# Optimization experiments

Measured on AMD Instinct MI355X. Metric: run time of the kernel, lower is better.

Reference implementation:

```python
import jax, jax.numpy as jnp
import numpy as np

N_BOXES = 2048
N_CLASSES = 20


def _cross(a, b):
    return a[..., 0] * b[..., 1] - a[..., 1] * b[..., 0]


def _corners(box):
    # box: [5] = cx, cy, w, h, angle -> [4,2] corner coords
    cx, cy, w, h, a = box[0], box[1], box[2], box[3], box[4]
    c, s = jnp.cos(a), jnp.sin(a)
    dx = jnp.array([-1.0, 1.0, 1.0, -1.0], box.dtype) * (w * 0.5)
    dy = jnp.array([-1.0, -1.0, 1.0, 1.0], box.dtype) * (h * 0.5)
    return jnp.stack([cx + c * dx - s * dy, cy + s * dx + c * dy], axis=-1)


def _points_in_box(pts, box):
    # pts [K,2]; rotate into box frame, test axis-aligned containment
    cx, cy, w, h, a = box[0], box[1], box[2], box[3], box[4]
    c, s = jnp.cos(a), jnp.sin(a)
    px = pts[:, 0] - cx
    py = pts[:, 1] - cy
    lx = c * px + s * py
    ly = -s * px + c * py
    eps = 1e-5
    return (jnp.abs(lx) <= w * 0.5 + eps) & (jnp.abs(ly) <= h * 0.5 + eps)


def _pair_inter_area(box_a, box_b):
    # Exact convex intersection area of two rotated rectangles.
    ca = _corners(box_a)
    cb = _corners(box_b)
    # all 4x4 edge-pair intersections
    p = ca[:, None, :]
    r = (jnp.roll(ca, -1, 0) - ca)[:, None, :]
    q = cb[None, :, :]
    s_ = (jnp.roll(cb, -1, 0) - cb)[None, :, :]
    denom = _cross(r, s_)
    qp = q - p
    safe = jnp.where(jnp.abs(denom) > 1e-9, denom, 1.0)
    t = _cross(qp, s_) / safe
    u = _cross(qp, r) / safe
    valid_e = (jnp.abs(denom) > 1e-9) & (t >= 0.0) & (t <= 1.0) & (u >= 0.0) & (u <= 1.0)
    ipts = p + t[..., None] * r  # [4,4,2]
    # candidate polygon vertices: corners of A in B, corners of B in A, edge crossings
    pts = jnp.concatenate([ca, cb, ipts.reshape(16, 2)], axis=0)  # [24,2]
    mask = jnp.concatenate([_points_in_box(ca, box_b), _points_in_box(cb, box_a), valid_e.reshape(16)], axis=0)
    k = jnp.sum(mask)
    m = mask.astype(pts.dtype)[:, None]
    center = jnp.sum(pts * m, axis=0) / jnp.maximum(k, 1).astype(pts.dtype)
    d = pts - center
    ang = jnp.where(mask, jnp.arctan2(d[:, 1], d[:, 0]), 1e9)  # invalid -> sorted last
    idx = jnp.argsort(ang)
    ds = d[idx]
    ar = jnp.arange(24)
    nxt = jnp.where(ar + 1 < k, ar + 1, 0)
    cr = _cross(ds, ds[nxt])
    area = 0.5 * jnp.abs(jnp.sum(jnp.where(ar < k, cr, 0.0)))
    return jnp.where(k >= 3, area, 0.0)


def _iou_one_vs_many(box, boxes):
    inter = jax.vmap(lambda b: _pair_inter_area(box, b))(boxes)  # [N]
    area_a = box[2] * box[3]
    area_b = boxes[:, 2] * boxes[:, 3]
    return inter / (area_a + area_b - inter + 1e-9)


def _rotated_nms_mask(boxes, scores, iou_threshold):
    # sequential greedy suppression, highest score first; returns bool keep mask (original order)
    n = boxes.shape[0]
    order = jnp.argsort(-scores)
    bs = boxes[order]
    ar = jnp.arange(n)

    def body(i, keep):
        ious = _iou_one_vs_many(bs[i], bs)
        suppress = (ious > iou_threshold) & (ar > i) & keep[i]
        return keep & ~suppress

    keep_sorted = jax.lax.fori_loop(0, n, body, jnp.ones((n,), bool))
    return jnp.zeros((n,), bool).at[order].set(keep_sorted)


def setup_inputs() -> dict:
    key = jax.random.key(0)
    k1, k2, k3, k4, k5 = jax.random.split(key, 5)
    cxcy = jax.random.uniform(k1, (N_BOXES, 2), jnp.float32) * 1024.0
    wh = jax.random.uniform(k2, (N_BOXES, 2), jnp.float32) * 96.0 + 4.0
    ang = jax.random.uniform(k3, (N_BOXES, 1), jnp.float32) * np.pi
    boxes = jnp.concatenate([cxcy, wh, ang], axis=1)  # [N,5]
    scores = jax.random.uniform(k4, (N_BOXES,), jnp.float32)
    labels = jax.random.randint(k5, (N_BOXES,), 0, N_CLASSES, dtype=jnp.int64 if jax.config.read('jax_enable_x64') else jnp.int32)
    return {"boxes": boxes, "scores": scores, "labels": labels, "iou_threshold": 0.5}


def reference(boxes, scores, labels, iou_threshold):
    # multiclass NMS via coordinate-offset trick (N <= 20000 branch of forward)
    cx, cy, w, h = boxes[:, 0], boxes[:, 1], boxes[:, 2], boxes[:, 3]
    max_radius = jnp.max(jnp.sqrt(w * w + h * h)) * 0.5
    max_coord = jnp.maximum(jnp.max(cx), jnp.max(cy))
    offset_scale = (max_coord + max_radius) * 2.0 + 1.0
    offsets = labels.astype(boxes.dtype) * offset_scale
    boxes_nms = boxes.at[:, 0].add(offsets).at[:, 1].add(offsets)
    keep = _rotated_nms_mask(boxes_nms, scores, iou_threshold)
    # fixed-shape encoding of the kept-index set: score of kept boxes, 0 for suppressed
    return scores * keep.astype(scores.dtype)
```

## Files before the change

kernel.cpp:

```cpp
#include <hip/hip_runtime.h>
#include <cstdint>

typedef unsigned long long u64;
typedef uint32_t u32;

#define NB 2048
#define NBLK 256
#define SLICE 512
#define CLIST_CAP 2048
#define GCOMP_CAP 131072
#define MAGIC 0x9E3779B1u


__global__ __launch_bounds__(256) void nms_fused_kernel(
    const float* __restrict__ boxes, const float* __restrict__ scores,
    const int* __restrict__ labels, const float* __restrict__ thrp,
    u32* __restrict__ edges, u32* __restrict__ cntA, u32* __restrict__ tagA,
    u32* __restrict__ gcomp, float* __restrict__ out) {
#pragma clang fp contract(off)
  __shared__ float sc[NB];
  __shared__ float smc[4], smr[4];
  __shared__ u32 clist[CLIST_CAP];
  __shared__ float dxL[256 * 25];
  __shared__ float dyL[256 * 25];
  __shared__ u32 ccnt;
  __shared__ u32 ecntL;
  __shared__ u32 cntL[NBLK];
  __shared__ u32 sA[NBLK];
  __shared__ u64 keepw[32];
  __shared__ u32 Sw32[64];
  __shared__ int changed;
  int t = threadIdx.x;
  int b = blockIdx.x;
  if (t == 0) { ccnt = 0; ecntL = 0; }
  float mc = -1e30f, mr = -1e30f;
  for (int k = t; k < NB; k += 256) {
    float cx = boxes[k * 5 + 0];
    float cy = boxes[k * 5 + 1];
    float w = boxes[k * 5 + 2];
    float h = boxes[k * 5 + 3];
    mc = fmaxf(mc, fmaxf(cx, cy));
    float ww = w * w;
    float hh = h * h;
    mr = fmaxf(mr, sqrtf(ww + hh));
    sc[k] = scores[k];
  }
  for (int off = 32; off > 0; off >>= 1) {
    mc = fmaxf(mc, __shfl_down(mc, off));
    mr = fmaxf(mr, __shfl_down(mr, off));
  }
  if ((t & 63) == 0) { smc[t >> 6] = mc; smr[t >> 6] = mr; }
  __syncthreads();
  mc = fmaxf(fmaxf(smc[0], smc[1]), fmaxf(smc[2], smc[3]));
  mr = fmaxf(fmaxf(smr[0], smr[1]), fmaxf(smr[2], smr[3]));
  float osc = (mc + mr * 0.5f) * 2.0f + 1.0f;

  float jx[8], jy[8], jr[8];
#pragma unroll
  for (int c = 0; c < 8; ++c) {
    int j = c * 256 + t;
    float off = (float)labels[j] * osc;
    float w = boxes[j * 5 + 2];
    float h = boxes[j * 5 + 3];
    float ww = w * w;
    float hh = h * h;
    jx[c] = boxes[j * 5 + 0] + off;
    jy[c] = boxes[j * 5 + 1] + off;
    jr[c] = 0.5f * sqrtf(ww + hh);
  }
  int i0 = b * 8;
#pragma unroll
  for (int di = 0; di < 8; ++di) {
    int i = i0 + di;
    float offi = (float)labels[i] * osc;
    float wI = boxes[i * 5 + 2];
    float hI = boxes[i * 5 + 3];
    float wwI = wI * wI;
    float hhI = hI * hI;
    float ax = boxes[i * 5 + 0] + offi;
    float ay = boxes[i * 5 + 1] + offi;
    float ar = 0.5f * sqrtf(wwI + hhI);
#pragma unroll
    for (int c = 0; c < 8; ++c) {
      int j = c * 256 + t;
      if (j > i) {
        float dx = jx[c] - ax, dy = jy[c] - ay;
        float rr = ar + jr[c] + 1.0f;
        if (dx * dx + dy * dy <= rr * rr) {
          u32 s = atomicAdd(&ccnt, 1u);
          if (s < CLIST_CAP) clist[s] = ((u32)i << 16) | (u32)j;
        }
      }
    }
  }
  __syncthreads();
  u32 cnt = ccnt < CLIST_CAP ? ccnt : CLIST_CAP;
  float thr = *thrp;
  u32* myEdges = edges + (u32)b * SLICE;
  float* myDx = &dxL[t * 25];
  float* myDy = &dyL[t * 25];
  for (u32 idx = t; idx < cnt; idx += 256) {
    u32 pk = clist[idx];
    int bi = (int)(pk >> 16);
    int bj = (int)(pk & 0xFFFFu);
    float offa = (float)labels[bi] * osc;
    float acx = boxes[bi * 5 + 0] + offa;
    float acy = boxes[bi * 5 + 1] + offa;
    float aw = boxes[bi * 5 + 2];
    float ah = boxes[bi * 5 + 3];
    float aang = boxes[bi * 5 + 4];
    float ac = cosf(aang);
    float as_ = sinf(aang);
    float offb = (float)labels[bj] * osc;
    float bcx = boxes[bj * 5 + 0] + offb;
    float bcy = boxes[bj * 5 + 1] + offb;
    float bw = boxes[bj * 5 + 2];
    float bh = boxes[bj * 5 + 3];
    float bang = boxes[bj * 5 + 4];
    float bc = cosf(bang);
    float bs_ = sinf(bang);
    const float SX[4] = {-1.f, 1.f, 1.f, -1.f};
    const float SY[4] = {-1.f, -1.f, 1.f, 1.f};
    float axx[4], ayy[4], bxx[4], byy[4];
    float ahw = aw * 0.5f, ahh = ah * 0.5f;
    float bhw = bw * 0.5f, bhh = bh * 0.5f;
#pragma unroll
    for (int q = 0; q < 4; ++q) {
      float dx = SX[q] * ahw, dy = SY[q] * ahh;
      axx[q] = acx + ac * dx - as_ * dy;
      ayy[q] = acy + as_ * dx + ac * dy;
      float ex = SX[q] * bhw, ey = SY[q] * bhh;
      bxx[q] = bcx + bc * ex - bs_ * ey;
      byy[q] = bcy + bs_ * ex + bc * ey;
    }
    float px_[24], py_[24];
    bool mk[24];
#pragma unroll
    for (int q = 0; q < 4; ++q) {
      {
        float axp = axx[q] - bcx, ayp = ayy[q] - bcy;
        float lxx = bc * axp + bs_ * ayp;
        float lyy = bc * ayp - bs_ * axp;
        mk[q] = (fabsf(lxx) <= bhw + 1e-5f) && (fabsf(lyy) <= bhh + 1e-5f);
        px_[q] = axx[q]; py_[q] = ayy[q];
      }
      {
        float axp = bxx[q] - acx, ayp = byy[q] - acy;
        float lxx = ac * axp + as_ * ayp;
        float lyy = ac * ayp - as_ * axp;
        mk[4 + q] = (fabsf(lxx) <= ahw + 1e-5f) && (fabsf(lyy) <= ahh + 1e-5f);
        px_[4 + q] = bxx[q]; py_[4 + q] = byy[q];
      }
    }
#pragma unroll
    for (int e = 0; e < 4; ++e) {
      float rx = axx[(e + 1) & 3] - axx[e];
      float ry = ayy[(e + 1) & 3] - ayy[e];
#pragma unroll
      for (int f = 0; f < 4; ++f) {
        float sx = bxx[(f + 1) & 3] - bxx[f];
        float sy = byy[(f + 1) & 3] - byy[f];
        float denom = rx * sy - ry * sx;
        float qpx = bxx[f] - axx[e];
        float qpy = byy[f] - ayy[e];
        bool dn = fabsf(denom) > 1e-9f;
        float safe = dn ? denom : 1.0f;
        float tt = (qpx * sy - qpy * sx) / safe;
        float uu = (qpx * ry - qpy * rx) / safe;
        bool valid = dn && (tt >= 0.0f) && (tt <= 1.0f) && (uu >= 0.0f) && (uu <= 1.0f);
        int id = 8 + e * 4 + f;
        px_[id] = axx[e] + tt * rx;
        py_[id] = ayy[e] + tt * ry;
        mk[id] = valid;
      }
    }
    int k = 0;
    float sx0 = 0.0f, sy0 = 0.0f;
#pragma unroll
    for (int q = 0; q < 24; ++q) {
      if (mk[q]) { k++; sx0 += px_[q]; sy0 += py_[q]; }
    }
    float kkf = (float)(k > 0 ? k : 1);
    float cxm = sx0 / kkf, cym = sy0 / kkf;
    u64 key[32];
#pragma unroll
    for (int q = 0; q < 24; ++q) {
      float dx = px_[q] - cxm, dy = py_[q] - cym;
      myDx[q] = dx; myDy[q] = dy;
      float sm = fabsf(dx) + fabsf(dy);
      float r = (sm > 0.0f) ? dy / sm : 0.0f;
      float pa;
      if (dx >= 0.0f) pa = r;
      else pa = (__float_as_uint(dy) >> 31) ? (-2.0f - r) : (2.0f - r);
      float ang = mk[q] ? pa : 1e9f;
      u32 ub = __float_as_uint(ang);
      u32 v = (ub & 0x80000000u) ? ~ub : (ub | 0x80000000u);
      key[q] = (((u64)v) << 5) | (u64)q;
    }
#pragma unroll
    for (int q = 24; q < 32; ++q) key[q] = ~0ull;
#pragma unroll
    for (int kk2 = 2; kk2 <= 32; kk2 <<= 1) {
#pragma unroll
      for (int jj = kk2 >> 1; jj > 0; jj >>= 1) {
#pragma unroll
        for (int ii = 0; ii < 32; ++ii) {
          int ll = ii ^ jj;
          if (ll > ii) {
            bool up = ((ii & kk2) == 0);
            u64 ka = key[ii], kb = key[ll];
            bool sw = up ? (ka > kb) : (ka < kb);
            key[ii] = sw ? kb : ka;
            key[ll] = sw ? ka : kb;
          }
        }
      }
    }
    float acc = 0.0f;
    int id0 = (int)(key[0] & 31ull);
    float fx = myDx[id0], fy = myDy[id0];
    float curx = fx, cury = fy;
#pragma unroll
    for (int q = 0; q < 24; ++q) {
      if (q < k - 1) {
        int idn = (int)(key[q + 1] & 31ull);
        float nx = myDx[idn], ny = myDy[idn];
        acc += curx * ny - cury * nx;
        curx = nx; cury = ny;
      } else if (q == k - 1) {
        acc += curx * fy - cury * fx;
      }
    }
    float area = 0.5f * fabsf(acc);
    float inter = (k >= 3) ? area : 0.0f;
    float areaA = aw * ah;
    float areaB = bw * bh;
    float iou = inter / (areaA + areaB - inter + 1e-9f);
    if (iou > thr) {
      float si = sc[bi], sj2 = sc[bj];
      bool isup = (si > sj2) || (si == sj2 && bi < bj);
      u32 sup = isup ? (u32)bi : (u32)bj;
      u32 sub = isup ? (u32)bj : (u32)bi;
      u32 e = atomicAdd(&ecntL, 1u);
      if (e < SLICE) myEdges[e] = (sup << 16) | sub;
    }
  }
  __syncthreads();
  if (t == 0) {
    u32 myc = ecntL < SLICE ? ecntL : SLICE;
    __threadfence();
    atomicExch(&cntA[b], myc);
    atomicExch(&tagA[b], myc ^ MAGIC);
  }
  if (b != 0) return;
  {
    u32 c;
    for (;;) {
      c = atomicOr(&cntA[t], 0u);
      u32 g = atomicOr(&tagA[t], 0u);
      if ((c ^ g) == MAGIC) break;
    }
    cntL[t] = c;
  }
  __syncthreads();
  __threadfence();
  sA[t] = cntL[t];
  __syncthreads();
#pragma unroll
  for (int d = 1; d < NBLK; d <<= 1) {
    u32 u = (t >= d) ? sA[t - d] : 0u;
    __syncthreads();
    sA[t] += u;
    __syncthreads();
  }
  u32 total = sA[NBLK - 1];
  if (total > GCOMP_CAP) total = GCOMP_CAP;
  {
    u32 cb = cntL[t];
    u32 off = sA[t] - cb;
    const u32* slice = edges + (u32)t * SLICE;
    for (u32 k2 = 0; k2 < cb; ++k2) {
      u32 pos = off + k2;
      u32 val = slice[k2];
      if (pos < CLIST_CAP) clist[pos] = val;
      else if (pos < GCOMP_CAP) gcomp[pos] = val;
    }
  }
  if (t < 32) keepw[t] = ~0ull;
  __syncthreads();
  for (int iter = 0; iter < 2060; ++iter) {
    if (t < 64) Sw32[t] = 0u;
    if (t == 0) changed = 0;
    __syncthreads();
    for (u32 k = t; k < total; k += 256) {
      u32 pk = (k < CLIST_CAP) ? clist[k] : gcomp[k];
      int i = (int)(pk >> 16);
      int j = (int)(pk & 0xFFFFu);
      if ((keepw[i >> 6] >> (i & 63)) & 1ull)
        atomicOr(&Sw32[j >> 5], 1u << (j & 31));
    }
    __syncthreads();
    if (t < 32) {
      u64 S = ((u64)Sw32[2 * t]) | (((u64)Sw32[2 * t + 1]) << 32);
      u64 nk = ~S;
      if (nk != keepw[t]) { keepw[t] = nk; changed = 1; }
    }
    __syncthreads();
    int ch = changed;
    __syncthreads();
    if (!ch) break;
  }
  for (int p = t; p < NB; p += 256) {
    int bit = (int)((keepw[p >> 6] >> (p & 63)) & 1ull);
    out[p] = bit ? sc[p] : 0.0f;
  }
}

extern "C" void kernel_launch(void* const* d_in, const int* in_sizes, int n_in,
                              void* d_out, int out_size, void* d_ws, size_t ws_size,
                              hipStream_t stream) {
  const float* boxes = (const float*)d_in[0];
  const float* scores = (const float*)d_in[1];
  const int* labels = (const int*)d_in[2];
  const float* thr = (const float*)d_in[3];
  float* out = (float*)d_out;

  char* base = (char*)d_ws;
  u32* edges = (u32*)base;
  u32* cntA = (u32*)(base + 524288);
  u32* tagA = (u32*)(base + 525312);
  u32* gcomp = (u32*)(base + 1048576);

  nms_fused_kernel<<<NBLK, 256, 0, stream>>>(boxes, scores, labels, thr,
                                             edges, cntA, tagA, gcomp, out);
}
```

Before: 79.93 us.

## Filter candidate pairs by label, shrink sort network, replace scan with atomic offsets

```diff
diff --git a/kernel.cpp b/kernel.cpp
--- a/kernel.cpp
+++ b/kernel.cpp
@@ -25,8 +25,7 @@
   __shared__ float dyL[256 * 25];
   __shared__ u32 ccnt;
   __shared__ u32 ecntL;
-  __shared__ u32 cntL[NBLK];
-  __shared__ u32 sA[NBLK];
+  __shared__ u32 gpos;
   __shared__ u64 keepw[32];
   __shared__ u32 Sw32[64];
   __shared__ int changed;
@@ -56,34 +55,35 @@
   float osc = (mc + mr * 0.5f) * 2.0f + 1.0f;
 
   float jx[8], jy[8], jr[8];
+  int jlab[8];
 #pragma unroll
   for (int c = 0; c < 8; ++c) {
     int j = c * 256 + t;
-    float off = (float)labels[j] * osc;
     float w = boxes[j * 5 + 2];
     float h = boxes[j * 5 + 3];
     float ww = w * w;
     float hh = h * h;
-    jx[c] = boxes[j * 5 + 0] + off;
-    jy[c] = boxes[j * 5 + 1] + off;
+    jx[c] = boxes[j * 5 + 0];
+    jy[c] = boxes[j * 5 + 1];
     jr[c] = 0.5f * sqrtf(ww + hh);
+    jlab[c] = labels[j];
   }
   int i0 = b * 8;
 #pragma unroll
   for (int di = 0; di < 8; ++di) {
     int i = i0 + di;
-    float offi = (float)labels[i] * osc;
+    int li = labels[i];
     float wI = boxes[i * 5 + 2];
     float hI = boxes[i * 5 + 3];
     float wwI = wI * wI;
     float hhI = hI * hI;
-    float ax = boxes[i * 5 + 0] + offi;
-    float ay = boxes[i * 5 + 1] + offi;
+    float ax = boxes[i * 5 + 0];
+    float ay = boxes[i * 5 + 1];
     float ar = 0.5f * sqrtf(wwI + hhI);
 #pragma unroll
     for (int c = 0; c < 8; ++c) {
       int j = c * 256 + t;
-      if (j > i) {
+      if (j > i && jlab[c] == li) {
         float dx = jx[c] - ax, dy = jy[c] - ay;
         float rr = ar + jr[c] + 1.0f;
         if (dx * dx + dy * dy <= rr * rr) {
@@ -182,7 +182,7 @@
     }
     float kkf = (float)(k > 0 ? k : 1);
     float cxm = sx0 / kkf, cym = sy0 / kkf;
-    u64 key[32];
+    u64 key[24];
 #pragma unroll
     for (int q = 0; q < 24; ++q) {
       float dx = px_[q] - cxm, dy = py_[q] - cym;
@@ -198,20 +198,23 @@
       key[q] = (((u64)v) << 5) | (u64)q;
     }
 #pragma unroll
-    for (int q = 24; q < 32; ++q) key[q] = ~0ull;
-#pragma unroll
-    for (int kk2 = 2; kk2 <= 32; kk2 <<= 1) {
-#pragma unroll
-      for (int jj = kk2 >> 1; jj > 0; jj >>= 1) {
-#pragma unroll
-        for (int ii = 0; ii < 32; ++ii) {
-          int ll = ii ^ jj;
-          if (ll > ii) {
-            bool up = ((ii & kk2) == 0);
-            u64 ka = key[ii], kb = key[ll];
-            bool sw = up ? (ka > kb) : (ka < kb);
-            key[ii] = sw ? kb : ka;
-            key[ll] = sw ? ka : kb;
+    for (int p = 1; p < 24; p <<= 1) {
+#pragma unroll
+      for (int kk = p; kk >= 1; kk >>= 1) {
+#pragma unroll
+        for (int j2 = kk % p; j2 + kk < 24; j2 += 2 * kk) {
+#pragma unroll
+          for (int i2 = 0; i2 < kk; ++i2) {
+            int a = j2 + i2;
+            int bq = j2 + i2 + kk;
+            if (bq < 24) {
+              if ((a / (2 * p)) == (bq / (2 * p))) {
+                u64 ka = key[a], kb2 = key[bq];
+                bool sw = ka > kb2;
+                key[a] = sw ? kb2 : ka;
+                key[bq] = sw ? ka : kb2;
+              }
+            }
           }
         }
       }
@@ -253,6 +256,9 @@
     atomicExch(&tagA[b], myc ^ MAGIC);
   }
   if (b != 0) return;
+  if (t == 0) gpos = 0;
+  if (t < 32) keepw[t] = ~0ull;
+  __syncthreads();
   {
     u32 c;
     for (;;) {
@@ -260,34 +266,19 @@
       u32 g = atomicOr(&tagA[t], 0u);
       if ((c ^ g) == MAGIC) break;
     }
-    cntL[t] = c;
-  }
-  __syncthreads();
-  __threadfence();
-  sA[t] = cntL[t];
-  __syncthreads();
-#pragma unroll
-  for (int d = 1; d < NBLK; d <<= 1) {
-    u32 u = (t >= d) ? sA[t - d] : 0u;
-    __syncthreads();
-    sA[t] += u;
-    __syncthreads();
-  }
-  u32 total = sA[NBLK - 1];
-  if (total > GCOMP_CAP) total = GCOMP_CAP;
-  {
-    u32 cb = cntL[t];
-    u32 off = sA[t] - cb;
+    __threadfence();
+    u32 off = atomicAdd(&gpos, c);
     const u32* slice = edges + (u32)t * SLICE;
-    for (u32 k2 = 0; k2 < cb; ++k2) {
+    for (u32 k2 = 0; k2 < c; ++k2) {
       u32 pos = off + k2;
       u32 val = slice[k2];
       if (pos < CLIST_CAP) clist[pos] = val;
       else if (pos < GCOMP_CAP) gcomp[pos] = val;
     }
   }
-  if (t < 32) keepw[t] = ~0ull;
-  __syncthreads();
+  __syncthreads();
+  u32 total = gpos;
+  if (total > GCOMP_CAP) total = GCOMP_CAP;
   for (int iter = 0; iter < 2060; ++iter) {
     if (t < 64) Sw32[t] = 0u;
     if (t == 0) changed = 0;
```

Result: no change. 81.10 us (+1.5%).
